# Kernel tuning notes

Measured on AMD Instinct MI355X. Metric: run time of the kernel, lower is better.

Reference implementation:

```python
import jax, jax.numpy as jnp
import numpy as np

N = 50000      # nodes
E = 800000     # edges (before self loops)
C = 128        # channels (in = out per head)
H = 4          # heads (concat=False -> mean over heads)
ALPHA = 0.2    # residual blend weight
NEG_SLOPE = 0.2  # GATConv default leaky_relu slope


def setup_inputs() -> dict:
    key = jax.random.key(0)
    k = jax.random.split(key, 6)
    x = jax.random.normal(k[0], (N, C), jnp.float32)
    edge_index = jax.random.randint(k[1], (2, E), 0, N, jnp.int32)
    # GATConv params: shared linear to H*C, per-head attention vectors, output bias
    W = jax.random.normal(k[2], (C, H * C), jnp.float32) / np.sqrt(C).astype(np.float32)
    att_src = jax.random.normal(k[3], (H, C), jnp.float32) / np.sqrt(C).astype(np.float32)
    att_dst = jax.random.normal(k[4], (H, C), jnp.float32) / np.sqrt(C).astype(np.float32)
    bias = jnp.zeros((C,), jnp.float32)
    return dict(x=x, edge_index=edge_index, W=W, att_src=att_src, att_dst=att_dst, bias=bias)


def reference(x, edge_index, W, att_src, att_dst, bias):
    # add self loops (PyG GATConv default add_self_loops=True)
    loops = jnp.arange(N, dtype=edge_index.dtype)
    src = jnp.concatenate([edge_index[0], loops])  # source / message sender j
    dst = jnp.concatenate([edge_index[1], loops])  # destination / receiver i

    xh = (x @ W).reshape(N, H, C)                      # [N,H,C] per-head features
    a_src = jnp.einsum('nhc,hc->nh', xh, att_src)      # [N,H]
    a_dst = jnp.einsum('nhc,hc->nh', xh, att_dst)      # [N,H]

    e = a_src[src] + a_dst[dst]                        # [E+N,H] raw scores
    e = jnp.where(e > 0, e, NEG_SLOPE * e)             # leaky_relu

    # destination-grouped softmax (every node has a self loop -> no empty segments)
    m = jax.ops.segment_max(e, dst, num_segments=N)    # [N,H]
    m = jnp.where(jnp.isfinite(m), m, 0.0)
    p = jnp.exp(e - m[dst])
    s = jax.ops.segment_sum(p, dst, num_segments=N)    # [N,H]
    w = p / (s[dst] + 1e-16)                           # [E+N,H] attention weights

    # scatter-add weighted messages
    out = jax.ops.segment_sum(w[:, :, None] * xh[src], dst, num_segments=N)  # [N,H,C]
    refined = out.mean(axis=1) + bias                  # concat=False -> head mean

    return (1.0 - ALPHA) * x + ALPHA * refined
```

## Files before the change

### kernel.cpp

```cpp
#include <hip/hip_runtime.h>
#include <math.h>

#define NN 50000
#define EE 800000
#define TOT (EE + NN)
#define CC 128
#define HH 4
#define HCW 512
#define SCAN_B 196
#define RB 64
#define GEMB ((NN + RB - 1) / RB)
#define CNTB ((TOT + 1023) / 1024)
#define LOG2E 1.442695040888963f

typedef short s16x8 __attribute__((ext_vector_type(8)));
typedef float f32x4 __attribute__((ext_vector_type(4)));
typedef float f32x2 __attribute__((ext_vector_type(2)));

__device__ __forceinline__ unsigned f2bf(float f) {
    unsigned u = __float_as_uint(f);
    return (u + 0x7fffu + ((u >> 16) & 1u)) >> 16;
}

__global__ __launch_bounds__(256) void k_prep_w(
    const float* __restrict__ W, unsigned short* __restrict__ wt)
{
    const int i = blockIdx.x * 256 + threadIdx.x;
    if (i >= HCW * CC) return;
    const int c = i >> 7, k = i & 127;
    wt[i] = (unsigned short)f2bf(W[(size_t)k * HCW + c]);
}

__global__ __launch_bounds__(1024, 4) void k_fat(
    const float* __restrict__ x,
    const unsigned short* __restrict__ wt,
    const float* __restrict__ att_s, const float* __restrict__ att_d,
    const int* __restrict__ ei,
    unsigned char* __restrict__ xhq,
    float* __restrict__ asrc, float* __restrict__ adst,
    int* __restrict__ deg, unsigned short* __restrict__ pos)
{
    __shared__ unsigned short xs[RB][CC + 8];
    __shared__ float red[16][2][16];

    if (blockIdx.x >= GEMB) {
        const int e = (blockIdx.x - GEMB) * 1024 + threadIdx.x;
        if (e < TOT) {
            const int d = (e < EE) ? ei[EE + e] : (e - EE);
            pos[e] = (unsigned short)atomicAdd(deg + d, 1);
        }
        return;
    }

    const int r0   = blockIdx.x * RB;
    const int wv   = threadIdx.x >> 6;
    const int lane = threadIdx.x & 63;
    const int lrow = lane & 15;
    const int kg   = lane >> 4;
    const int n_base = wv * 32;
    const int h    = wv >> 2;

    for (int i = threadIdx.x; i < RB * 32; i += 1024) {
        const int row = i >> 5;
        const int c4  = (i & 31) * 4;
        const int grow = r0 + row;
        float4 v = make_float4(0.f, 0.f, 0.f, 0.f);
        if (grow < NN) v = *(const float4*)(x + (size_t)grow * CC + c4);
        uint2 o;
        o.x = f2bf(v.x) | (f2bf(v.y) << 16);
        o.y = f2bf(v.z) | (f2bf(v.w) << 16);
        *(uint2*)(&xs[row][c4]) = o;
    }

    s16x8 wf0[4], wf1[4];
#pragma unroll
    for (int kk = 0; kk < 4; ++kk) {
        wf0[kk] = *(const s16x8*)(wt + (size_t)(n_base + 0  + lrow) * CC + kg * 8 + kk * 32);
        wf1[kk] = *(const s16x8*)(wt + (size_t)(n_base + 16 + lrow) * CC + kg * 8 + kk * 32);
    }
    __syncthreads();

    const int cbase = h * CC + (wv & 3) * 32 + kg * 4;

    for (int rt = 0; rt < 4; ++rt) {
        f32x4 acc0 = {0.f, 0.f, 0.f, 0.f};
        f32x4 acc1 = {0.f, 0.f, 0.f, 0.f};
#pragma unroll
        for (int kk = 0; kk < 4; ++kk) {
            const s16x8 b = *(const s16x8*)(&xs[rt * 16 + lrow][kg * 8 + kk * 32]);
            acc0 = __builtin_amdgcn_mfma_f32_16x16x32_bf16(wf0[kk], b, acc0, 0, 0, 0);
            acc1 = __builtin_amdgcn_mfma_f32_16x16x32_bf16(wf1[kk], b, acc1, 0, 0, 0);
        }

        const int grow = r0 + rt * 16 + lrow;
        if (grow < NN) {
            unsigned char* orow = xhq + (size_t)grow * HCW + n_base + kg * 4;
            unsigned u;
            u = __builtin_amdgcn_cvt_pk_fp8_f32(acc0[0], acc0[1], 0u, false);
            u = __builtin_amdgcn_cvt_pk_fp8_f32(acc0[2], acc0[3], u, true);
            *(unsigned*)(orow) = u;
            u = __builtin_amdgcn_cvt_pk_fp8_f32(acc1[0], acc1[1], 0u, false);
            u = __builtin_amdgcn_cvt_pk_fp8_f32(acc1[2], acc1[3], u, true);
            *(unsigned*)(orow + 16) = u;
        }

        float ps, pd;
        {
            const float4 c0 = *(const float4*)(att_s + cbase);
            const float4 c1 = *(const float4*)(att_s + cbase + 16);
            ps = acc0[0]*c0.x + acc0[1]*c0.y + acc0[2]*c0.z + acc0[3]*c0.w
               + acc1[0]*c1.x + acc1[1]*c1.y + acc1[2]*c1.z + acc1[3]*c1.w;
        }
        {
            const float4 c0 = *(const float4*)(att_d + cbase);
            const float4 c1 = *(const float4*)(att_d + cbase + 16);
            pd = acc0[0]*c0.x + acc0[1]*c0.y + acc0[2]*c0.z + acc0[3]*c0.w
               + acc1[0]*c1.x + acc1[1]*c1.y + acc1[2]*c1.z + acc1[3]*c1.w;
        }
        ps += __shfl_xor(ps, 16); ps += __shfl_xor(ps, 32);
        pd += __shfl_xor(pd, 16); pd += __shfl_xor(pd, 32);
        red[wv][0][lrow] = ps;
        red[wv][1][lrow] = pd;
        __syncthreads();
        if (threadIdx.x < 128) {
            const int t     = threadIdx.x & 15;
            const int hh    = (threadIdx.x >> 4) & 3;
            const int which = threadIdx.x >> 6;
            const int row   = r0 + rt * 16 + t;
            if (row < NN) {
                const float v = red[hh * 4 + 0][which][t] + red[hh * 4 + 1][which][t]
                              + red[hh * 4 + 2][which][t] + red[hh * 4 + 3][which][t];
                float* dst = which ? adst : asrc;
                dst[row * HH + hh] = v * LOG2E;
            }
        }
        __syncthreads();
    }
}

__global__ __launch_bounds__(256) void s_part(
    const int* __restrict__ deg, int* __restrict__ part)
{
    const int idx = blockIdx.x * 256 + threadIdx.x;
    int v = (idx < NN) ? deg[idx] : 0;
#pragma unroll
    for (int off = 1; off < 64; off <<= 1) v += __shfl_xor(v, off);
    __shared__ int sm[4];
    if ((threadIdx.x & 63) == 0) sm[threadIdx.x >> 6] = v;
    __syncthreads();
    if (threadIdx.x == 0) part[blockIdx.x] = sm[0] + sm[1] + sm[2] + sm[3];
}

__global__ __launch_bounds__(256) void s_apply(
    const int* __restrict__ deg, const int* __restrict__ part,
    int* __restrict__ rowptr)
{
    __shared__ int sm[256];
    __shared__ int ws[4];
    const int t   = threadIdx.x;
    const int bid = blockIdx.x;

    int pv = (t < SCAN_B && t < bid) ? part[t] : 0;
#pragma unroll
    for (int off = 1; off < 64; off <<= 1) pv += __shfl_xor(pv, off);
    if ((t & 63) == 0) ws[t >> 6] = pv;
    __syncthreads();
    const int poff = ws[0] + ws[1] + ws[2] + ws[3];

    const int idx = bid * 256 + t;
    const int v = (idx < NN) ? deg[idx] : 0;
    sm[t] = v;
    __syncthreads();
    for (int off = 1; off < 256; off <<= 1) {
        int u = (t >= off) ? sm[t - off] : 0;
        __syncthreads();
        sm[t] += u;
        __syncthreads();
    }
    if (idx < NN) rowptr[idx] = poff + sm[t] - v;
    if (bid == 0 && t == 0) rowptr[NN] = TOT;
}

__global__ __launch_bounds__(256) void k_scatter(
    const int* __restrict__ ei, const int* __restrict__ rowptr,
    const unsigned short* __restrict__ pos, int* __restrict__ csr_s)
{
    const int e = blockIdx.x * 256 + threadIdx.x;
    if (e >= TOT) return;
    int s, d;
    if (e < EE) { s = ei[e]; d = ei[EE + e]; } else { s = d = e - EE; }
    csr_s[rowptr[d] + pos[e]] = s;
}

__global__ __launch_bounds__(256) void k_gather(
    const int* __restrict__ rowptr, const int* __restrict__ csr_s,
    const float* __restrict__ asrc, const float* __restrict__ adst,
    const unsigned char* __restrict__ xhq, const float* __restrict__ x,
    const float* __restrict__ bias, float* __restrict__ out)
{
    const int gtid = blockIdx.x * 256 + threadIdx.x;
    const int n    = __builtin_amdgcn_readfirstlane(gtid >> 6);
    const int lane = threadIdx.x & 63;
    if (n >= NN) return;
    const int h = lane >> 4;
    const int t = lane & 15;

    const int beg = __builtin_amdgcn_readfirstlane(rowptr[n]);
    const int end = __builtin_amdgcn_readfirstlane(rowptr[n + 1]);
    const float ad = adst[n * HH + h];
    const int voff = lane << 3;

    float ssum = 0.f;
    f32x2 a0 = {0.f, 0.f}, a1 = {0.f, 0.f}, a2 = {0.f, 0.f}, a3 = {0.f, 0.f};

    int j = beg;
    for (; j + 8 <= end; j += 8) {
        int ss[8];
#pragma unroll
        for (int u = 0; u < 8; ++u)
            ss[u] = __builtin_amdgcn_readfirstlane(csr_s[j + u]);
        uint2 qq[8];
#pragma unroll
        for (int u = 0; u < 8; ++u)
            qq[u] = *(const uint2*)(xhq + ((size_t)(unsigned)ss[u] << 9) + voff);
        float ww[8];
#pragma unroll
        for (int u = 0; u < 8; ++u) {
            float e = asrc[(ss[u] << 2) + h] + ad;
            e = fmaxf(e, 0.2f * e);
            ww[u] = exp2f(e);
            ssum += ww[u];
        }
#pragma unroll
        for (int u = 0; u < 8; ++u) {
            const f32x2 p0 = __builtin_amdgcn_cvt_pk_f32_fp8(qq[u].x, false);
            const f32x2 p1 = __builtin_amdgcn_cvt_pk_f32_fp8(qq[u].x, true);
            const f32x2 p2 = __builtin_amdgcn_cvt_pk_f32_fp8(qq[u].y, false);
            const f32x2 p3 = __builtin_amdgcn_cvt_pk_f32_fp8(qq[u].y, true);
            const f32x2 wv = {ww[u], ww[u]};
            a0 += wv * p0; a1 += wv * p1; a2 += wv * p2; a3 += wv * p3;
        }
    }
    for (int base = j; base < end; base += 4) {
        int ss[4];
#pragma unroll
        for (int u = 0; u < 4; ++u) {
            const int idx = (base + u < end) ? (base + u) : (end - 1);
            ss[u] = __builtin_amdgcn_readfirstlane(csr_s[idx]);
        }
        uint2 qq[4];
#pragma unroll
        for (int u = 0; u < 4; ++u)
            qq[u] = *(const uint2*)(xhq + ((size_t)(unsigned)ss[u] << 9) + voff);
        float ww[4];
#pragma unroll
        for (int u = 0; u < 4; ++u) {
            float e = asrc[(ss[u] << 2) + h] + ad;
            e = fmaxf(e, 0.2f * e);
            float w = exp2f(e);
            w = (base + u < end) ? w : 0.f;
            ww[u] = w;
            ssum += w;
        }
#pragma unroll
        for (int u = 0; u < 4; ++u) {
            const f32x2 p0 = __builtin_amdgcn_cvt_pk_f32_fp8(qq[u].x, false);
            const f32x2 p1 = __builtin_amdgcn_cvt_pk_f32_fp8(qq[u].x, true);
            const f32x2 p2 = __builtin_amdgcn_cvt_pk_f32_fp8(qq[u].y, false);
            const f32x2 p3 = __builtin_amdgcn_cvt_pk_f32_fp8(qq[u].y, true);
            const f32x2 wv = {ww[u], ww[u]};
            a0 += wv * p0; a1 += wv * p1; a2 += wv * p2; a3 += wv * p3;
        }
    }

    const float inv = 0.25f / (ssum + 1e-16f);
    const f32x2 iv = {inv, inv};
    a0 *= iv; a1 *= iv; a2 *= iv; a3 *= iv;
    float r0 = a0.x, r1 = a0.y, r2 = a1.x, r3 = a1.y;
    float r4 = a2.x, r5 = a2.y, r6 = a3.x, r7 = a3.y;

#pragma unroll
    for (int off = 16; off < 64; off <<= 1) {
        r0 += __shfl_xor(r0, off); r1 += __shfl_xor(r1, off);
        r2 += __shfl_xor(r2, off); r3 += __shfl_xor(r3, off);
        r4 += __shfl_xor(r4, off); r5 += __shfl_xor(r5, off);
        r6 += __shfl_xor(r6, off); r7 += __shfl_xor(r7, off);
    }

    if (h == 0) {
        const int c = t * 8;
        const float4 x0 = *(const float4*)(x + (size_t)n * CC + c);
        const float4 x1 = *(const float4*)(x + (size_t)n * CC + c + 4);
        const float4 b0 = *(const float4*)(bias + c);
        const float4 b1 = *(const float4*)(bias + c + 4);
        float4 o0, o1;
        o0.x = 0.8f * x0.x + 0.2f * (r0 + b0.x);
        o0.y = 0.8f * x0.y + 0.2f * (r1 + b0.y);
        o0.z = 0.8f * x0.z + 0.2f * (r2 + b0.z);
        o0.w = 0.8f * x0.w + 0.2f * (r3 + b0.w);
        o1.x = 0.8f * x1.x + 0.2f * (r4 + b1.x);
        o1.y = 0.8f * x1.y + 0.2f * (r5 + b1.y);
        o1.z = 0.8f * x1.z + 0.2f * (r6 + b1.z);
        o1.w = 0.8f * x1.w + 0.2f * (r7 + b1.w);
        *(float4*)(out + (size_t)n * CC + c)     = o0;
        *(float4*)(out + (size_t)n * CC + c + 4) = o1;
    }
}

extern "C" void kernel_launch(void* const* d_in, const int* in_sizes, int n_in,
                              void* d_out, int out_size, void* d_ws, size_t ws_size,
                              hipStream_t stream)
{
    const float* x     = (const float*)d_in[0];
    const int*   ei    = (const int*)d_in[1];
    const float* W     = (const float*)d_in[2];
    const float* att_s = (const float*)d_in[3];
    const float* att_d = (const float*)d_in[4];
    const float* bias  = (const float*)d_in[5];
    float* out = (float*)d_out;

    char* p = (char*)d_ws;
    unsigned char*  xhq   = (unsigned char*)p;  p += (size_t)NN * HCW;
    unsigned short* wt    = (unsigned short*)p; p += (size_t)HCW * CC * 2;
    float*          asrc  = (float*)p;          p += (size_t)NN * HH * 4;
    float*          adst  = (float*)p;          p += (size_t)NN * HH * 4;
    int*            deg   = (int*)p;            p += (size_t)NN * 4;
    unsigned short* pos   = (unsigned short*)p; p += (size_t)TOT * 2;
    int*            rowptr= (int*)p;            p += (size_t)(NN + 1) * 4;
    int*            csr_s = (int*)p;            p += (size_t)TOT * 4;
    int*            part  = (int*)p;            p += (size_t)SCAN_B * 4;

    hipMemsetAsync(deg, 0, (size_t)NN * 4, stream);

    k_prep_w<<<(HCW * CC + 255) / 256, 256, 0, stream>>>(W, wt);
    k_fat<<<GEMB + CNTB, 1024, 0, stream>>>(x, wt, att_s, att_d, ei, xhq, asrc, adst, deg, pos);
    s_part<<<SCAN_B, 256, 0, stream>>>(deg, part);
    s_apply<<<SCAN_B, 256, 0, stream>>>(deg, part, rowptr);
    k_scatter<<<(TOT + 255) / 256, 256, 0, stream>>>(ei, rowptr, pos, csr_s);
    {
        const long long threads = (long long)NN * 64;
        const int blocks = (int)((threads + 255) / 256);
        k_gather<<<blocks, 256, 0, stream>>>(rowptr, csr_s, asrc, adst, xhq, x, bias, out);
    }
}
```

Measured before the change: 162.8 us.

## Batch attention reductions, reorder fused blocks, deepen gather unroll to 16

In the fused GEMM/degree-count kernel, the atomic degree-counting blocks now come first in the grid, so they are scheduled before the GEMM blocks. The per-row-tile attention reduction, which needed two block barriers per tile, is replaced by one shared-memory reduction after all four tiles, leaving a single barrier. In the gather kernel the main edge loop is unrolled from 8 to 16 edges to keep more independent loads in flight. Each edge's source score is now read as one float4 and the head value picked with selects, instead of a scalar indexed load. The wider unroll raises register pressure, which may lower occupancy.

```diff
diff --git a/kernel.cpp b/kernel.cpp
--- a/kernel.cpp
+++ b/kernel.cpp
@@ -41,10 +41,10 @@
     int* __restrict__ deg, unsigned short* __restrict__ pos)
 {
     __shared__ unsigned short xs[RB][CC + 8];
-    __shared__ float red[16][2][16];
-
-    if (blockIdx.x >= GEMB) {
-        const int e = (blockIdx.x - GEMB) * 1024 + threadIdx.x;
+    __shared__ float red[16][2][4][16];
+
+    if (blockIdx.x < CNTB) {
+        const int e = blockIdx.x * 1024 + threadIdx.x;
         if (e < TOT) {
             const int d = (e < EE) ? ei[EE + e] : (e - EE);
             pos[e] = (unsigned short)atomicAdd(deg + d, 1);
@@ -52,7 +52,7 @@
         return;
     }
 
-    const int r0   = blockIdx.x * RB;
+    const int r0   = (blockIdx.x - CNTB) * RB;
     const int wv   = threadIdx.x >> 6;
     const int lane = threadIdx.x & 63;
     const int lrow = lane & 15;
@@ -82,6 +82,8 @@
 
     const int cbase = h * CC + (wv & 3) * 32 + kg * 4;
 
+    float psr[4], pdr[4];
+
     for (int rt = 0; rt < 4; ++rt) {
         f32x4 acc0 = {0.f, 0.f, 0.f, 0.f};
         f32x4 acc1 = {0.f, 0.f, 0.f, 0.f};
@@ -119,22 +121,28 @@
         }
         ps += __shfl_xor(ps, 16); ps += __shfl_xor(ps, 32);
         pd += __shfl_xor(pd, 16); pd += __shfl_xor(pd, 32);
-        red[wv][0][lrow] = ps;
-        red[wv][1][lrow] = pd;
-        __syncthreads();
-        if (threadIdx.x < 128) {
-            const int t     = threadIdx.x & 15;
-            const int hh    = (threadIdx.x >> 4) & 3;
-            const int which = threadIdx.x >> 6;
-            const int row   = r0 + rt * 16 + t;
-            if (row < NN) {
-                const float v = red[hh * 4 + 0][which][t] + red[hh * 4 + 1][which][t]
-                              + red[hh * 4 + 2][which][t] + red[hh * 4 + 3][which][t];
-                float* dst = which ? adst : asrc;
-                dst[row * HH + hh] = v * LOG2E;
-            }
-        }
-        __syncthreads();
+        psr[rt] = ps;
+        pdr[rt] = pd;
+    }
+
+#pragma unroll
+    for (int rt = 0; rt < 4; ++rt) {
+        red[wv][0][rt][lrow] = psr[rt];
+        red[wv][1][rt][lrow] = pdr[rt];
+    }
+    __syncthreads();
+    if (threadIdx.x < 512) {
+        const int t     = threadIdx.x & 15;
+        const int rt    = (threadIdx.x >> 4) & 3;
+        const int hh    = (threadIdx.x >> 6) & 3;
+        const int which = (threadIdx.x >> 8) & 1;
+        const int row   = r0 + rt * 16 + t;
+        if (row < NN) {
+            const float v = red[hh * 4 + 0][which][rt][t] + red[hh * 4 + 1][which][rt][t]
+                          + red[hh * 4 + 2][which][rt][t] + red[hh * 4 + 3][which][rt][t];
+            float* dst = which ? adst : asrc;
+            dst[row * HH + hh] = v * LOG2E;
+        }
     }
 }
 
@@ -204,35 +212,40 @@
     if (n >= NN) return;
     const int h = lane >> 4;
     const int t = lane & 15;
+    const bool hb0 = (h & 1) != 0;
+    const bool hb1 = (h & 2) != 0;
 
     const int beg = __builtin_amdgcn_readfirstlane(rowptr[n]);
     const int end = __builtin_amdgcn_readfirstlane(rowptr[n + 1]);
     const float ad = adst[n * HH + h];
     const int voff = lane << 3;
+    const float4* asrc4 = (const float4*)asrc;
 
     float ssum = 0.f;
     f32x2 a0 = {0.f, 0.f}, a1 = {0.f, 0.f}, a2 = {0.f, 0.f}, a3 = {0.f, 0.f};
 
     int j = beg;
-    for (; j + 8 <= end; j += 8) {
-        int ss[8];
-#pragma unroll
-        for (int u = 0; u < 8; ++u)
+    for (; j + 16 <= end; j += 16) {
+        int ss[16];
+#pragma unroll
+        for (int u = 0; u < 16; ++u)
             ss[u] = __builtin_amdgcn_readfirstlane(csr_s[j + u]);
-        uint2 qq[8];
-#pragma unroll
-        for (int u = 0; u < 8; ++u)
+        uint2 qq[16];
+#pragma unroll
+        for (int u = 0; u < 16; ++u)
             qq[u] = *(const uint2*)(xhq + ((size_t)(unsigned)ss[u] << 9) + voff);
-        float ww[8];
-#pragma unroll
-        for (int u = 0; u < 8; ++u) {
-            float e = asrc[(ss[u] << 2) + h] + ad;
+        float ww[16];
+#pragma unroll
+        for (int u = 0; u < 16; ++u) {
+            const float4 av = asrc4[ss[u]];
+            float e = hb1 ? (hb0 ? av.w : av.z) : (hb0 ? av.y : av.x);
+            e += ad;
             e = fmaxf(e, 0.2f * e);
             ww[u] = exp2f(e);
             ssum += ww[u];
         }
 #pragma unroll
-        for (int u = 0; u < 8; ++u) {
+        for (int u = 0; u < 16; ++u) {
             const f32x2 p0 = __builtin_amdgcn_cvt_pk_f32_fp8(qq[u].x, false);
             const f32x2 p1 = __builtin_amdgcn_cvt_pk_f32_fp8(qq[u].x, true);
             const f32x2 p2 = __builtin_amdgcn_cvt_pk_f32_fp8(qq[u].y, false);
@@ -255,7 +268,9 @@
         float ww[4];
 #pragma unroll
         for (int u = 0; u < 4; ++u) {
-            float e = asrc[(ss[u] << 2) + h] + ad;
+            const float4 av = asrc4[ss[u]];
+            float e = hb1 ? (hb0 ? av.w : av.z) : (hb0 ? av.y : av.x);
+            e += ad;
             e = fmaxf(e, 0.2f * e);
             float w = exp2f(e);
             w = (base + u < end) ? w : 0.f;
@@ -333,7 +348,7 @@
     hipMemsetAsync(deg, 0, (size_t)NN * 4, stream);
 
     k_prep_w<<<(HCW * CC + 255) / 256, 256, 0, stream>>>(W, wt);
-    k_fat<<<GEMB + CNTB, 1024, 0, stream>>>(x, wt, att_s, att_d, ei, xhq, asrc, adst, deg, pos);
+    k_fat<<<CNTB + GEMB, 1024, 0, stream>>>(x, wt, att_s, att_d, ei, xhq, asrc, adst, deg, pos);
     s_part<<<SCAN_B, 256, 0, stream>>>(deg, part);
     s_apply<<<SCAN_B, 256, 0, stream>>>(deg, part, rowptr);
     k_scatter<<<(TOT + 255) / 256, 256, 0, stream>>>(ei, rowptr, pos, csr_s);
```

Measured after the change: 183.1 us. 1.12x slower.
